# Kernel tuning notes

Hardware: AMD Instinct MI355X
Metric: run time of the kernel (lower is better)

The kernel has to match this reference:

```python
import jax, jax.numpy as jnp
import numpy as np

N_PART = 2048
N_BINS = 16
N_FREQS = 8
N_BLOCKS = 4
N_HEADS = 8
DIM = 256
HID = 512
LOWER = 0.0
UPPER = 1.0
FIXED_IDXS = np.array([0, 1])
CHANGED_IDXS = np.array([2])
N_FIXED = 2
N_CHANGED = 1
EMB_IN = 2 * N_FREQS * N_FIXED + 3   # 35
AFF_OUT = N_CHANGED * (3 * N_BINS + 1)  # 49
MIN_BIN = 1e-4
MIN_SLOPE = 1e-4


def _mlp(x, W0, b0, W1, b1, W2, b2):
    # equinox MLP: depth=2 hidden layers, relu activation, identity final
    x = jax.nn.relu(x @ W0.T + b0)
    x = jax.nn.relu(x @ W1.T + b1)
    return x @ W2.T + b2


def _attention(x, Wq, Wk, bk, Wv, Wo, bo):
    # eqx.nn.MultiheadAttention: query bias off, key bias on, value bias off, output bias on
    S, D = x.shape
    dh = D // N_HEADS
    q = (x @ Wq.T).reshape(S, N_HEADS, dh)
    k = (x @ Wk.T + bk).reshape(S, N_HEADS, dh)
    v = (x @ Wv.T).reshape(S, N_HEADS, dh)
    logits = jnp.einsum('shd,thd->hst', q, k) / float(np.sqrt(dh))
    attn = jax.nn.softmax(logits, axis=-1)
    o = jnp.einsum('hst,thd->shd', attn, v).reshape(S, D)
    return o @ Wo.T + bo


def _circular(x, lower, upper, n_freqs):
    # periodic sin/cos embedding of coordinates on [lower, upper)
    freqs = 2.0 * jnp.pi * jnp.arange(1, n_freqs + 1, dtype=x.dtype) / (upper - lower)
    ang = (x - lower)[..., None] * freqs  # (rows, n_fixed, n_freqs)
    feats = jnp.concatenate([jnp.cos(ang), jnp.sin(ang)], axis=-1)
    return feats.reshape(x.shape[0], -1)  # (rows, 2*n_freqs*n_fixed)


def _rqs_forward(x, params):
    # distrax-style rational quadratic spline, boundary_slopes='circular'
    nb = N_BINS
    uw = params[..., :nb]
    uh = params[..., nb:2 * nb]
    ud = params[..., 2 * nb:]
    ud = jnp.concatenate([ud[..., :-1], ud[..., :1]], axis=-1)  # circular: last slope = first
    total = UPPER - LOWER
    widths = jax.nn.softmax(uw, axis=-1) * (total - nb * MIN_BIN) + MIN_BIN
    heights = jax.nn.softmax(uh, axis=-1) * (total - nb * MIN_BIN) + MIN_BIN
    offset = float(np.log(np.expm1(1.0 - MIN_SLOPE)))  # softplus(0+offset)+min = 1
    slopes = jax.nn.softplus(ud + offset) + MIN_SLOPE
    zero = jnp.zeros(widths.shape[:-1] + (1,), widths.dtype)
    xpos = LOWER + jnp.concatenate([zero, jnp.cumsum(widths, -1)], -1)   # (..., nb+1)
    ypos = LOWER + jnp.concatenate([zero, jnp.cumsum(heights, -1)], -1)
    inside = (x >= LOWER) & (x <= UPPER)
    xc = jnp.clip(x, LOWER, UPPER)
    k = jnp.clip(jnp.sum(xc[..., None] >= xpos, axis=-1) - 1, 0, nb - 1)
    g = lambda a: jnp.take_along_axis(a, k[..., None], axis=-1)[..., 0]
    xk, xk1 = g(xpos[..., :-1]), g(xpos[..., 1:])
    yk, yk1 = g(ypos[..., :-1]), g(ypos[..., 1:])
    dk, dk1 = g(slopes[..., :-1]), g(slopes[..., 1:])
    w = xk1 - xk
    h = yk1 - yk
    s = h / w
    z = (xc - xk) / w
    z1 = 1.0 - z
    den = s + (dk1 + dk - 2.0 * s) * z * z1
    y = yk + h * (s * z * z + dk * z * z1) / den
    logdet = 2.0 * jnp.log(s) + jnp.log(dk1 * z * z + 2.0 * s * z * z1 + dk * z1 * z1) - 2.0 * jnp.log(den)
    y = jnp.where(inside, y, x)
    logdet = jnp.where(inside, logdet, 0.0)
    return y, logdet


def _forward(pos, scale, press, temp,
             e_w0, e_b0, e_w1, e_b1, e_w2, e_b2,
             Wq, Wk, bk, Wv, Wo, bo,
             mw0, mb0, mw1, mb1, mw2, mb2,
             a_w0, a_b0, a_w1, a_b1, a_w2, a_b2):
    fixed = pos[1:, FIXED_IDXS]      # (N-1, 2)
    changed = pos[1:, CHANGED_IDXS]  # (N-1, 1)
    feats = _circular(fixed[:, FIXED_IDXS], LOWER, UPPER, N_FREQS)  # (N-1, 32)
    rows = feats.shape[0]
    ones = jnp.ones((rows, 1), feats.dtype)
    cond = jnp.concatenate([feats, ones * scale, ones * temp, ones * press], axis=-1)  # (N-1, 35)
    h = _mlp(cond, e_w0, e_b0, e_w1, e_b1, e_w2, e_b2)  # (N-1, DIM)
    for i in range(N_BLOCKS):
        h = h + _attention(h, Wq[i], Wk[i], bk[i], Wv[i], Wo[i], bo[i])
        h = h + _mlp(h, mw0[i], mb0[i], mw1[i], mb1[i], mw2[i], mb2[i])
    params = _mlp(h, a_w0, a_b0, a_w1, a_b1, a_w2, a_b2)
    params = params.reshape(N_PART - 1, N_CHANGED, 3 * N_BINS + 1)
    y, logdet = _rqs_forward(changed, params)
    pos = pos.at[1:, CHANGED_IDXS].set(y.reshape(N_PART - 1, N_CHANGED))
    return pos, logdet.sum()


def setup_inputs():
    kit = iter(jax.random.split(jax.random.key(0), 40))
    nk = lambda: next(kit)
    def W(out_d, in_d, pre=()):
        return jax.random.normal(nk(), pre + (out_d, in_d), jnp.float32) / np.sqrt(in_d)
    def b(out_d, pre=()):
        return 0.01 * jax.random.normal(nk(), pre + (out_d,), jnp.float32)
    B = (N_BLOCKS,)
    return dict(
        pos=jax.random.uniform(nk(), (N_PART, 3), jnp.float32),
        scale=jax.random.uniform(nk(), (), jnp.float32),
        press=jax.random.uniform(nk(), (), jnp.float32),
        temp=jax.random.uniform(nk(), (), jnp.float32),
        e_w0=W(HID, EMB_IN), e_b0=b(HID),
        e_w1=W(HID, HID), e_b1=b(HID),
        e_w2=W(DIM, HID), e_b2=b(DIM),
        Wq=W(DIM, DIM, B), Wk=W(DIM, DIM, B), bk=b(DIM, B),
        Wv=W(DIM, DIM, B), Wo=W(DIM, DIM, B), bo=b(DIM, B),
        mw0=W(HID, DIM, B), mb0=b(HID, B),
        mw1=W(HID, HID, B), mb1=b(HID, B),
        mw2=W(DIM, HID, B), mb2=b(DIM, B),
        a_w0=W(HID, DIM), a_b0=b(HID),
        a_w1=W(HID, HID), a_b1=b(HID),
        a_w2=W(AFF_OUT, HID), a_b2=b(AFF_OUT),
    )


def reference(pos, scale, press, temp,
              e_w0, e_b0, e_w1, e_b1, e_w2, e_b2,
              Wq, Wk, bk, Wv, Wo, bo,
              mw0, mb0, mw1, mb1, mw2, mb2,
              a_w0, a_b0, a_w1, a_b1, a_w2, a_b2):
    return _forward(pos, scale, press, temp,
                    e_w0, e_b0, e_w1, e_b1, e_w2, e_b2,
                    Wq, Wk, bk, Wv, Wo, bo,
                    mw0, mb0, mw1, mb1, mw2, mb2,
                    a_w0, a_b0, a_w1, a_b1, a_w2, a_b2)
```

## Files before the change

kernel.cpp:

```cpp
#include <hip/hip_runtime.h>
#include <math.h>

#define S_ROWS 2047
#define DIM 256
#define HID 512
#define NHEADS 8
#define DH 32
#define NBINS 16
#define AFF_OUT 49

typedef short bf16x8 __attribute__((ext_vector_type(8)));
typedef float f32x4 __attribute__((ext_vector_type(4)));
typedef float f32x16 __attribute__((ext_vector_type(16)));
typedef unsigned short u16x8 __attribute__((ext_vector_type(8)));
typedef unsigned short u16x4 __attribute__((ext_vector_type(4)));

__device__ inline unsigned short f2b(float f) {
    unsigned int u = __float_as_uint(f);
    u += 0x7FFFu + ((u >> 16) & 1u);
    return (unsigned short)(u >> 16);
}

#define W_MAIN 3957248
#define EW0P_N 32768
#define P0 (W_MAIN / 4)
#define P1 (P0 + EW0P_N / 4)
#define P2 (P1 + 2048 * 64 / 4)
#define P3 (P2 + 1537)
__global__ __launch_bounds__(256) void setup_kernel(
    const float* __restrict__ pos, const float* __restrict__ scale,
    const float* __restrict__ press, const float* __restrict__ temp,
    const float* __restrict__ e_w0, const float* __restrict__ p0,
    const float* __restrict__ p1, const float* __restrict__ p2,
    const float* __restrict__ p3, const float* __restrict__ p4,
    const float* __restrict__ p5, const float* __restrict__ p6,
    const float* __restrict__ p7, const float* __restrict__ p8,
    const float* __restrict__ p9, const float* __restrict__ p10,
    const float* __restrict__ p11, unsigned short* __restrict__ dst,
    unsigned short* __restrict__ cond, float* __restrict__ out)
{
    const int offs[13] = {0, 262144, 393216, 655360, 917504, 1179648, 1441792,
                          1966080, 3014656, 3538944, 3670016, 3932160, 3957248};
    const float* srcs[12] = {p0,p1,p2,p3,p4,p5,p6,p7,p8,p9,p10,p11};
    for (int i4 = blockIdx.x * blockDim.x + threadIdx.x; i4 < P3;
         i4 += gridDim.x * blockDim.x) {
        if (i4 < P0) {
            int e = i4 * 4;
            int s = 0;
            #pragma unroll
            for (int j = 1; j < 12; j++) s += (e >= offs[j]);
            const float4 v = *(const float4*)(srcs[s] + (e - offs[s]));
            u16x4 o;
            o[0] = f2b(v.x); o[1] = f2b(v.y); o[2] = f2b(v.z); o[3] = f2b(v.w);
            *(u16x4*)(dst + EW0P_N + e) = o;
        } else if (i4 < P1) {
            int e = (i4 - P0) * 4;
            u16x4 o;
            #pragma unroll
            for (int r = 0; r < 4; r++) {
                int ee = e + r;
                int row = ee >> 6, col = ee & 63;
                o[r] = (col < 35) ? f2b(e_w0[row * 35 + col]) : (unsigned short)0;
            }
            *(u16x4*)(dst + e) = o;
        } else if (i4 < P2) {
            int e = (i4 - P1) * 4;
            int row = e >> 6;
            u16x4 o;
            #pragma unroll
            for (int r = 0; r < 4; r++) {
                int c = (e + r) & 63;
                float v = 0.f;
                if (row < S_ROWS) {
                    if (c < 32) {
                        int coord = c >> 4;
                        int w = c & 15;
                        float x = pos[(row + 1) * 3 + coord];
                        float f = 6.283185307179586f * (float)((w & 7) + 1);
                        float ang = x * f;
                        v = (w < 8) ? cosf(ang) : sinf(ang);
                    } else if (c == 32) v = scale[0];
                    else if (c == 33) v = temp[0];
                    else if (c == 34) v = press[0];
                }
                o[r] = f2b(v);
            }
            *(u16x4*)(cond + e) = o;
        } else {
            int e = (i4 - P2) * 4;
            #pragma unroll
            for (int r = 0; r < 4; r++) {
                int ee = e + r;
                if (ee < 6144) out[ee] = pos[ee];
                else if (ee == 6144) out[ee] = 0.f;
            }
        }
    }
}

#define LDK 72
__global__ __launch_bounds__(256, 2) void gemm_bf16(
    const unsigned short* __restrict__ Ab, const unsigned short* __restrict__ W,
    const float* __restrict__ bias, const float* resF,
    float* Cf, unsigned short* Cb, int M, int K, int relu)
{
    __shared__ unsigned short As[64][LDK];
    __shared__ unsigned short Bs[32][LDK];
    int tid = threadIdx.x;
    int wave = tid >> 6, lane = tid & 63;
    int quad = lane >> 4, l16 = lane & 15;
    int row0 = blockIdx.y << 6, col0 = blockIdx.x << 5;
    int srow = tid >> 2, scol = (tid & 3) << 4;
    int srowB = tid >> 3, scolB = (tid & 7) << 3;

    f32x4 acc[2];
    #pragma unroll
    for (int i = 0; i < 2; i++) { f32x4 z = {0.f,0.f,0.f,0.f}; acc[i] = z; }

    const u16x8* ap = (const u16x8*)(Ab + (size_t)(row0 + srow) * K + scol);
    const u16x8* wp = (const u16x8*)(W + (size_t)(col0 + srowB) * K + scolB);
    u16x8 a0 = ap[0], a1 = ap[1];
    u16x8 b0 = wp[0];

    for (int k0 = 0; k0 < K; k0 += 64) {
        *(u16x8*)&As[srow][scol]     = a0;
        *(u16x8*)&As[srow][scol + 8] = a1;
        *(u16x8*)&Bs[srowB][scolB]   = b0;
        __syncthreads();
        if (k0 + 64 < K) {
            ap += 8; wp += 8;
            a0 = ap[0]; a1 = ap[1];
            b0 = wp[0];
        }
        #pragma unroll
        for (int kt = 0; kt < 64; kt += 32) {
            bf16x8 af = *(bf16x8*)&As[(wave << 4) + l16][kt + (quad << 3)];
            #pragma unroll
            for (int n0 = 0; n0 < 2; n0++) {
                bf16x8 bf = *(bf16x8*)&Bs[(n0 << 4) + l16][kt + (quad << 3)];
                acc[n0] = __builtin_amdgcn_mfma_f32_16x16x32_bf16(af, bf, acc[n0], 0, 0, 0);
            }
        }
        __syncthreads();
    }
    #pragma unroll
    for (int n0 = 0; n0 < 2; n0++) {
        int col = col0 + (n0 << 4) + l16;
        if (col >= M) continue;
        float bv = bias ? bias[col] : 0.f;
        #pragma unroll
        for (int r = 0; r < 4; r++) {
            int row = row0 + (wave << 4) + (quad << 2) + r;
            if (row >= S_ROWS) continue;
            float v = acc[n0][r] + bv;
            if (resF) v += resF[(size_t)row * M + col];
            if (relu) v = fmaxf(v, 0.f);
            if (Cf) Cf[(size_t)row * M + col] = v;
            if (Cb) Cb[(size_t)row * M + col] = f2b(v);
        }
    }
}

__global__ __launch_bounds__(256, 2) void gemm_qkv(
    const unsigned short* __restrict__ Ab, const unsigned short* __restrict__ Wq,
    const unsigned short* __restrict__ Wk, const unsigned short* __restrict__ Wv,
    const float* __restrict__ bk,
    unsigned short* __restrict__ qbh, unsigned short* __restrict__ kbh,
    unsigned short* __restrict__ vbT)
{
    __shared__ unsigned short As[64][LDK];
    __shared__ unsigned short Bs[32][LDK];
    const int N = S_ROWS, K = 256;
    int tid = threadIdx.x;
    int wave = tid >> 6, lane = tid & 63;
    int quad = lane >> 4, l16 = lane & 15;
    int row0 = blockIdx.y << 6, col0 = blockIdx.x << 5;
    int mode = col0 >> 8;
    int wcol0 = col0 & 255;
    const unsigned short* W = (mode == 0) ? Wq : (mode == 1) ? Wk : Wv;
    int srow = tid >> 2, scol = (tid & 3) << 4;
    int srowB = tid >> 3, scolB = (tid & 7) << 3;

    f32x4 acc[2];
    #pragma unroll
    for (int i = 0; i < 2; i++) { f32x4 z = {0.f,0.f,0.f,0.f}; acc[i] = z; }

    const u16x8* ap = (const u16x8*)(Ab + (size_t)(row0 + srow) * K + scol);
    const u16x8* wp = (const u16x8*)(W + (size_t)(wcol0 + srowB) * K + scolB);
    u16x8 a0 = ap[0], a1 = ap[1];
    u16x8 b0 = wp[0];

    for (int k0 = 0; k0 < K; k0 += 64) {
        *(u16x8*)&As[srow][scol]     = a0;
        *(u16x8*)&As[srow][scol + 8] = a1;
        *(u16x8*)&Bs[srowB][scolB]   = b0;
        __syncthreads();
        if (k0 + 64 < K) {
            ap += 8; wp += 8;
            a0 = ap[0]; a1 = ap[1];
            b0 = wp[0];
        }
        #pragma unroll
        for (int kt = 0; kt < 64; kt += 32) {
            bf16x8 af = *(bf16x8*)&As[(wave << 4) + l16][kt + (quad << 3)];
            #pragma unroll
            for (int n0 = 0; n0 < 2; n0++) {
                bf16x8 bf = *(bf16x8*)&Bs[(n0 << 4) + l16][kt + (quad << 3)];
                acc[n0] = __builtin_amdgcn_mfma_f32_16x16x32_bf16(af, bf, acc[n0], 0, 0, 0);
            }
        }
        __syncthreads();
    }
    #pragma unroll
    for (int n0 = 0; n0 < 2; n0++) {
        int colr = wcol0 + (n0 << 4) + l16;
        int hh = colr >> 5, d = colr & 31;
        int rbase = row0 + (wave << 4) + (quad << 2);
        if (mode == 2) {
            unsigned short* dst = vbT + ((size_t)hh * 32 + d) * 2048 + rbase;
            if (rbase + 3 < N) {
                u16x4 o;
                #pragma unroll
                for (int r = 0; r < 4; r++) o[r] = f2b(acc[n0][r]);
                *(u16x4*)dst = o;
            } else {
                #pragma unroll
                for (int r = 0; r < 4; r++)
                    if (rbase + r < N) dst[r] = f2b(acc[n0][r]);
            }
        } else {
            float bias = (mode == 1) ? bk[colr] : 0.f;
            unsigned short* dst = ((mode == 0) ? qbh : kbh) + (size_t)hh * 2048 * 32 + d;
            #pragma unroll
            for (int r = 0; r < 4; r++) {
                int row = rbase + r;
                if (row < N) {
                    float v = acc[n0][r] + bias;
                    if (mode == 0) v *= 0.25506362f;
                    dst[(size_t)row * 32] = f2b(v);
                }
            }
        }
    }
}

__global__ __launch_bounds__(256, 2) void attn_mfma(
    const unsigned short* __restrict__ qbh,
    const unsigned short* __restrict__ kbh,
    const unsigned short* __restrict__ vbT,
    unsigned short* __restrict__ obb)
{
    int tid = threadIdx.x;
    int w = tid >> 6;
    int lane = tid & 63;
    int l31 = lane & 31, hf = lane >> 5;
    int q0 = blockIdx.x << 5;
    int h = blockIdx.y;
    int kstart = w * 512;
    int kend = min(kstart + 512, S_ROWS);

    const unsigned short* qp = qbh + ((size_t)h * 2048 + (q0 + l31)) * 32 + hf * 8;
    bf16x8 qf0 = *(const bf16x8*)(qp);
    bf16x8 qf1 = *(const bf16x8*)(qp + 16);

    const unsigned short* kb_h = kbh + (size_t)h * 2048 * 32;
    const unsigned short* vb_h = vbT + ((size_t)h * 32 + l31) * 2048;

    f32x16 acc = {};
    float m = -1e30f, l = 0.f;

    for (int key0 = kstart; key0 < kend; key0 += 32) {
        const unsigned short* kp = kb_h + (size_t)(key0 + l31) * 32 + hf * 8;
        bf16x8 kf0 = *(const bf16x8*)(kp);
        bf16x8 kf1 = *(const bf16x8*)(kp + 16);
        bf16x8 vf0 = *(const bf16x8*)(vb_h + key0 + hf * 8);
        bf16x8 vf1 = *(const bf16x8*)(vb_h + key0 + 16 + hf * 8);

        f32x16 sc = {};
        sc = __builtin_amdgcn_mfma_f32_32x32x16_bf16(kf0, qf0, sc, 0, 0, 0);
        sc = __builtin_amdgcn_mfma_f32_32x32x16_bf16(kf1, qf1, sc, 0, 0, 0);

        if (key0 + 32 > kend) {
            #pragma unroll
            for (int r = 0; r < 16; r++) {
                int kr = key0 + (r & 3) + 8 * (r >> 2) + 4 * hf;
                if (kr >= kend) sc[r] = -1e30f;
            }
        }
        float tmax = sc[0];
        #pragma unroll
        for (int r = 1; r < 16; r++) tmax = fmaxf(tmax, sc[r]);
        tmax = fmaxf(tmax, __shfl_xor(tmax, 32, 64));
        float mnew = fmaxf(m, tmax);
        float corr = __builtin_amdgcn_exp2f(m - mnew);
        m = mnew;
        float p[16];
        float ls = 0.f;
        #pragma unroll
        for (int r = 0; r < 16; r++) {
            p[r] = __builtin_amdgcn_exp2f(sc[r] - mnew);
            ls += p[r];
        }
        ls += __shfl_xor(ls, 32, 64);
        l = l * corr + ls;
        if (__ballot(corr != 1.0f)) {
            #pragma unroll
            for (int r = 0; r < 16; r++) acc[r] *= corr;
        }
        unsigned int pk[8];
        #pragma unroll
        for (int i = 0; i < 8; i++)
            pk[i] = __builtin_amdgcn_perm(__float_as_uint(p[2*i+1]),
                                          __float_as_uint(p[2*i]), 0x07060302u);
        unsigned int x[8];
        #pragma unroll
        for (int i = 0; i < 8; i++)
            x[i] = (unsigned int)__shfl_xor((int)pk[i], 32, 64);
        union { unsigned int u[4]; bf16x8 v; } B1, B2;
        B1.u[0] = hf ? x[2]  : pk[0];
        B1.u[1] = hf ? x[3]  : pk[1];
        B1.u[2] = hf ? pk[2] : x[0];
        B1.u[3] = hf ? pk[3] : x[1];
        B2.u[0] = hf ? x[6]  : pk[4];
        B2.u[1] = hf ? x[7]  : pk[5];
        B2.u[2] = hf ? pk[6] : x[4];
        B2.u[3] = hf ? pk[7] : x[5];
        acc = __builtin_amdgcn_mfma_f32_32x32x16_bf16(vf0, B1.v, acc, 0, 0, 0);
        acc = __builtin_amdgcn_mfma_f32_32x32x16_bf16(vf1, B2.v, acc, 0, 0, 0);
    }

    __shared__ float sm_m[4][32];
    __shared__ float sm_l[4][32];
    __shared__ float sm_acc[4][32][36];
    if (!hf) { sm_m[w][l31] = m; sm_l[w][l31] = l; }
    #pragma unroll
    for (int g = 0; g < 4; g++) {
        float4 o4;
        o4.x = acc[4*g]; o4.y = acc[4*g+1]; o4.z = acc[4*g+2]; o4.w = acc[4*g+3];
        *(float4*)&sm_acc[w][l31][8*g + 4*hf] = o4;
    }
    __syncthreads();

    int q = tid & 31;
    int dg = tid >> 5;
    float mmax = fmaxf(fmaxf(sm_m[0][q], sm_m[1][q]),
                       fmaxf(sm_m[2][q], sm_m[3][q]));
    float lsum = 0.f;
    float num0 = 0.f, num1 = 0.f, num2 = 0.f, num3 = 0.f;
    #pragma unroll
    for (int c = 0; c < 4; c++) {
        float wgt = __builtin_amdgcn_exp2f(sm_m[c][q] - mmax);
        lsum += sm_l[c][q] * wgt;
        float4 o4 = *(const float4*)&sm_acc[c][q][dg * 4];
        num0 = fmaf(o4.x, wgt, num0);
        num1 = fmaf(o4.y, wgt, num1);
        num2 = fmaf(o4.z, wgt, num2);
        num3 = fmaf(o4.w, wgt, num3);
    }
    float inv = 1.f / lsum;
    if (q0 + q < S_ROWS) {
        u16x4 st;
        st[0] = f2b(num0 * inv); st[1] = f2b(num1 * inv);
        st[2] = f2b(num2 * inv); st[3] = f2b(num3 * inv);
        *(u16x4*)(obb + (size_t)(q0 + q) * DIM + h * DH + dg * 4) = st;
    }
}

__global__ __launch_bounds__(64) void spline_kernel(const float* __restrict__ pos,
    const float* __restrict__ params, float* __restrict__ out)
{
    int r = blockIdx.x * 64 + threadIdx.x;
    float ld = 0.f;
    if (r < S_ROWS) {
        const float* p = params + (size_t)r * AFF_OUT;
        float x = pos[(r + 1) * 3 + 2];
        float xc = fminf(fmaxf(x, 0.f), 1.f);

        float mw = -1e30f, mh = -1e30f;
        #pragma unroll
        for (int j = 0; j < NBINS; j++) {
            mw = fmaxf(mw, p[j]);
            mh = fmaxf(mh, p[NBINS + j]);
        }
        float sw = 0.f, sh = 0.f;
        #pragma unroll
        for (int j = 0; j < NBINS; j++) {
            sw += __expf(p[j] - mw);
            sh += __expf(p[NBINS + j] - mh);
        }
        const float span = 1.0f - NBINS * 1e-4f;
        float scw = span / sw, sch = span / sh;

        float cumw = 0.f, cumh = 0.f;
        float xk = 0.f, yk = 0.f, wk = 0.f, hk = 0.f;
        int k = 0;
        #pragma unroll
        for (int j = 0; j < NBINS; j++) {
            float wj = __expf(p[j] - mw) * scw + 1e-4f;
            float hj = __expf(p[NBINS + j] - mh) * sch + 1e-4f;
            if (xc >= cumw) { k = j; xk = cumw; yk = cumh; wk = wj; hk = hj; }
            cumw += wj; cumh += hj;
        }
        float offset = logf(expm1f(0.9999f));
        float t0 = p[2 * NBINS + k] + offset;
        float t1 = ((k == NBINS - 1) ? p[2 * NBINS] : p[2 * NBINS + k + 1]) + offset;
        float dk  = ((t0 > 15.f) ? t0 : log1pf(__expf(t0))) + 1e-4f;
        float dk1 = ((t1 > 15.f) ? t1 : log1pf(__expf(t1))) + 1e-4f;

        float sl = hk / wk;
        float z = (xc - xk) / wk;
        float z1 = 1.f - z;
        float den = sl + (dk1 + dk - 2.f * sl) * z * z1;
        float y = yk + hk * (sl * z * z + dk * z * z1) / den;
        float ldv = 2.f * logf(sl)
                  + logf(dk1 * z * z + 2.f * sl * z * z1 + dk * z1 * z1)
                  - 2.f * logf(den);
        bool inside = (x >= 0.f) && (x <= 1.f);
        y = inside ? y : x;
        ld = inside ? ldv : 0.f;
        out[(r + 1) * 3 + 2] = y;
    }
    #pragma unroll
    for (int st = 32; st > 0; st >>= 1) ld += __shfl_xor(ld, st, 64);
    if (threadIdx.x == 0) atomicAdd(&out[6144], ld);
}

extern "C" void kernel_launch(void* const* d_in, const int* in_sizes, int n_in,
                              void* d_out, int out_size, void* d_ws, size_t ws_size,
                              hipStream_t stream)
{
    const float* pos   = (const float*)d_in[0];
    const float* scale = (const float*)d_in[1];
    const float* press = (const float*)d_in[2];
    const float* temp  = (const float*)d_in[3];
    const float* e_w0  = (const float*)d_in[4];
    const float* e_b0  = (const float*)d_in[5];
    const float* e_w1  = (const float*)d_in[6];
    const float* e_b1  = (const float*)d_in[7];
    const float* e_w2  = (const float*)d_in[8];
    const float* e_b2  = (const float*)d_in[9];
    const float* Wq    = (const float*)d_in[10];
    const float* Wk    = (const float*)d_in[11];
    const float* bk    = (const float*)d_in[12];
    const float* Wv    = (const float*)d_in[13];
    const float* Wo    = (const float*)d_in[14];
    const float* bo    = (const float*)d_in[15];
    const float* mw0   = (const float*)d_in[16];
    const float* mb0   = (const float*)d_in[17];
    const float* mw1   = (const float*)d_in[18];
    const float* mb1   = (const float*)d_in[19];
    const float* mw2   = (const float*)d_in[20];
    const float* mb2   = (const float*)d_in[21];
    const float* a_w0  = (const float*)d_in[22];
    const float* a_b0  = (const float*)d_in[23];
    const float* a_w1  = (const float*)d_in[24];
    const float* a_b1  = (const float*)d_in[25];
    const float* a_w2  = (const float*)d_in[26];
    const float* a_b2  = (const float*)d_in[27];
    float* out = (float*)d_out;

    enum { OFF_EW0 = 0,
           OFF_EW1 = 32768 + 0,       OFF_EW2 = 32768 + 262144,
           OFF_WQ  = 32768 + 393216,  OFF_WK  = 32768 + 655360,
           OFF_WV  = 32768 + 917504,  OFF_WO  = 32768 + 1179648,
           OFF_MW0 = 32768 + 1441792, OFF_MW1 = 32768 + 1966080,
           OFF_MW2 = 32768 + 3014656, OFF_AW0 = 32768 + 3538944,
           OFF_AW1 = 32768 + 3670016, OFF_AW2 = 32768 + 3932160 };
    const size_t WB_U16 = (size_t)EW0P_N + W_MAIN;

    float* ws = (float*)d_ws;
    size_t off = 0;
    float* hbuf = ws + off; off += 2048 * 256;
    float* pr   = ws + off; off += 2048 * 64;
    unsigned short* wbp   = (unsigned short*)(ws + off); off += WB_U16 / 2;
    unsigned short* cond  = (unsigned short*)(ws + off); off += 2048 * 64 / 2;
    unsigned short* t1b   = (unsigned short*)(ws + off); off += 2048 * 512 / 2;
    unsigned short* t2b   = (unsigned short*)(ws + off); off += 2048 * 512 / 2;
    unsigned short* hb    = (unsigned short*)(ws + off); off += 2048 * 256 / 2;
    unsigned short* obb   = (unsigned short*)(ws + off); off += 2048 * 256 / 2;
    unsigned short* qbh   = (unsigned short*)(ws + off); off += NHEADS * 2048 * 32 / 2;
    unsigned short* kbh   = (unsigned short*)(ws + off); off += NHEADS * 2048 * 32 / 2;
    unsigned short* vbT   = (unsigned short*)(ws + off); off += NHEADS * 2048 * 32 / 2;
    (void)ws_size;

    dim3 b256(256);
    hipLaunchKernelGGL(setup_kernel, dim3(1024), b256, 0, stream,
                       pos, scale, press, temp, e_w0,
                       e_w1, e_w2, Wq, Wk, Wv, Wo, mw0, mw1, mw2,
                       a_w0, a_w1, a_w2, wbp, cond, out);

    auto gemm = [&](const unsigned short* A, const unsigned short* W,
                    const float* bias, const float* resF, float* Cf,
                    unsigned short* Cb, int M, int K, int relu) {
        dim3 grid((M + 31) / 32, 32);
        hipLaunchKernelGGL(gemm_bf16, grid, dim3(256), 0, stream,
                           A, W, bias, resF, Cf, Cb, M, K, relu);
    };

    gemm(cond, wbp + OFF_EW0, e_b0, nullptr, nullptr, t1b, 512, 64, 1);
    gemm(t1b,  wbp + OFF_EW1, e_b1, nullptr, nullptr, t2b, 512, 512, 1);
    gemm(t2b,  wbp + OFF_EW2, e_b2, nullptr, hbuf, hb, 256, 512, 0);

    for (int l = 0; l < 4; l++) {
        hipLaunchKernelGGL(gemm_qkv, dim3(24, 32), b256, 0, stream,
                           hb, wbp + OFF_WQ + l * 65536, wbp + OFF_WK + l * 65536,
                           wbp + OFF_WV + l * 65536, bk + l * 256, qbh, kbh, vbT);
        hipLaunchKernelGGL(attn_mfma, dim3(64, NHEADS), b256, 0, stream,
                           qbh, kbh, vbT, obb);
        gemm(obb, wbp + OFF_WO + l * 65536, bo + l * 256, hbuf, hbuf, hb, 256, 256, 0);
        gemm(hb,  wbp + OFF_MW0 + l * 131072, mb0 + l * 512, nullptr, nullptr, t1b, 512, 256, 1);
        gemm(t1b, wbp + OFF_MW1 + l * 262144, mb1 + l * 512, nullptr, nullptr, t2b, 512, 512, 1);
        gemm(t2b, wbp + OFF_MW2 + l * 131072, mb2 + l * 256, hbuf, hbuf, hb, 256, 512, 0);
    }

    gemm(hb,  wbp + OFF_AW0, a_b0, nullptr, nullptr, t1b, 512, 256, 1);
    gemm(t1b, wbp + OFF_AW1, a_b1, nullptr, nullptr, t2b, 512, 512, 1);
    gemm(t2b, wbp + OFF_AW2, a_b2, nullptr, pr, nullptr, AFF_OUT, 512, 0);

    hipLaunchKernelGGL(spline_kernel, dim3(32), dim3(64), 0, stream, pos, pr, out);
}
```

Before: 359.8 us.

## Fuse per-row MLP chains into single LDS-resident kernel per layer

Replaces the separate tiled GEMM launches (embedding MLP, QKV projection, output projection, block MLP, affine MLP, spline) with one chain kernel. Each 16-row block keeps activations and the residual stream in shared memory across consecutive linear layers, and streams weights directly from global memory into MFMA operands. This cuts kernel launches and the global round-trips of intermediate activations, leaving only attention as a separate kernel. In exchange, only 128 blocks of 512 threads run, and weights are re-read by every block without LDS staging, which may lower occupancy and raise weight traffic.

Result: slower. 441.2 us (+22.6%).

```diff
diff --git a/kernel.cpp b/kernel.cpp
--- a/kernel.cpp
+++ b/kernel.cpp
@@ -20,6 +20,20 @@
     u += 0x7FFFu + ((u >> 16) & 1u);
     return (unsigned short)(u >> 16);
 }
+
+#define OFF_EW0 0
+#define OFF_EW1 (32768 + 0)
+#define OFF_EW2 (32768 + 262144)
+#define OFF_WQ  (32768 + 393216)
+#define OFF_WK  (32768 + 655360)
+#define OFF_WV  (32768 + 917504)
+#define OFF_WO  (32768 + 1179648)
+#define OFF_MW0 (32768 + 1441792)
+#define OFF_MW1 (32768 + 1966080)
+#define OFF_MW2 (32768 + 3014656)
+#define OFF_AW0 (32768 + 3538944)
+#define OFF_AW1 (32768 + 3670016)
+#define OFF_AW2 (32768 + 3932160)
 
 #define W_MAIN 3957248
 #define EW0P_N 32768
@@ -98,135 +112,78 @@
     }
 }
 
-#define LDK 72
-__global__ __launch_bounds__(256, 2) void gemm_bf16(
-    const unsigned short* __restrict__ Ab, const unsigned short* __restrict__ W,
-    const float* __restrict__ bias, const float* resF,
-    float* Cf, unsigned short* Cb, int M, int K, int relu)
-{
-    __shared__ unsigned short As[64][LDK];
-    __shared__ unsigned short Bs[32][LDK];
-    int tid = threadIdx.x;
-    int wave = tid >> 6, lane = tid & 63;
-    int quad = lane >> 4, l16 = lane & 15;
-    int row0 = blockIdx.y << 6, col0 = blockIdx.x << 5;
-    int srow = tid >> 2, scol = (tid & 3) << 4;
-    int srowB = tid >> 3, scolB = (tid & 7) << 3;
-
-    f32x4 acc[2];
-    #pragma unroll
-    for (int i = 0; i < 2; i++) { f32x4 z = {0.f,0.f,0.f,0.f}; acc[i] = z; }
-
-    const u16x8* ap = (const u16x8*)(Ab + (size_t)(row0 + srow) * K + scol);
-    const u16x8* wp = (const u16x8*)(W + (size_t)(col0 + srowB) * K + scolB);
-    u16x8 a0 = ap[0], a1 = ap[1];
-    u16x8 b0 = wp[0];
-
-    for (int k0 = 0; k0 < K; k0 += 64) {
-        *(u16x8*)&As[srow][scol]     = a0;
-        *(u16x8*)&As[srow][scol + 8] = a1;
-        *(u16x8*)&Bs[srowB][scolB]   = b0;
-        __syncthreads();
-        if (k0 + 64 < K) {
-            ap += 8; wp += 8;
-            a0 = ap[0]; a1 = ap[1];
-            b0 = wp[0];
-        }
-        #pragma unroll
-        for (int kt = 0; kt < 64; kt += 32) {
-            bf16x8 af = *(bf16x8*)&As[(wave << 4) + l16][kt + (quad << 3)];
-            #pragma unroll
-            for (int n0 = 0; n0 < 2; n0++) {
-                bf16x8 bf = *(bf16x8*)&Bs[(n0 << 4) + l16][kt + (quad << 3)];
-                acc[n0] = __builtin_amdgcn_mfma_f32_16x16x32_bf16(af, bf, acc[n0], 0, 0, 0);
-            }
-        }
-        __syncthreads();
-    }
-    #pragma unroll
-    for (int n0 = 0; n0 < 2; n0++) {
-        int col = col0 + (n0 << 4) + l16;
-        if (col >= M) continue;
-        float bv = bias ? bias[col] : 0.f;
+#define LDA 520
+#define LDR 260
+
+template<int K, bool RELU, int RESMODE>
+__device__ inline void stage_lds(
+    const unsigned short (*IN)[LDA], unsigned short (*OUT)[LDA],
+    float (*res)[LDR],
+    const unsigned short* __restrict__ W, const float* __restrict__ bias,
+    int M, int wave, int quad, int l16)
+{
+    bf16x8 af[K / 32];
+    #pragma unroll
+    for (int i = 0; i < K / 32; i++)
+        af[i] = *(const bf16x8*)&IN[l16][(i << 5) + (quad << 3)];
+    for (int m0 = wave << 4; m0 < M; m0 += 128) {
+        const unsigned short* wp = W + (size_t)(m0 + l16) * K + (quad << 3);
+        f32x4 acc = {0.f, 0.f, 0.f, 0.f};
+        #pragma unroll
+        for (int i = 0; i < K / 32; i++) {
+            bf16x8 bf = *(const bf16x8*)(wp + (i << 5));
+            acc = __builtin_amdgcn_mfma_f32_16x16x32_bf16(af[i], bf, acc, 0, 0, 0);
+        }
+        int col = m0 + l16;
+        float bv = bias[col];
         #pragma unroll
         for (int r = 0; r < 4; r++) {
-            int row = row0 + (wave << 4) + (quad << 2) + r;
-            if (row >= S_ROWS) continue;
-            float v = acc[n0][r] + bv;
-            if (resF) v += resF[(size_t)row * M + col];
-            if (relu) v = fmaxf(v, 0.f);
-            if (Cf) Cf[(size_t)row * M + col] = v;
-            if (Cb) Cb[(size_t)row * M + col] = f2b(v);
-        }
-    }
-}
-
-__global__ __launch_bounds__(256, 2) void gemm_qkv(
-    const unsigned short* __restrict__ Ab, const unsigned short* __restrict__ Wq,
-    const unsigned short* __restrict__ Wk, const unsigned short* __restrict__ Wv,
-    const float* __restrict__ bk,
+            int row = (quad << 2) + r;
+            float v = acc[r] + bv;
+            if (RESMODE == 1) { v += res[row][col]; res[row][col] = v; }
+            if (RESMODE == 2) { res[row][col] = v; }
+            if (RELU) v = fmaxf(v, 0.f);
+            OUT[row][col] = f2b(v);
+        }
+    }
+}
+
+__device__ inline void stage_qkv(
+    const unsigned short (*IN)[LDA],
+    const unsigned short* __restrict__ Wq, const unsigned short* __restrict__ Wk,
+    const unsigned short* __restrict__ Wv, const float* __restrict__ bk,
     unsigned short* __restrict__ qbh, unsigned short* __restrict__ kbh,
-    unsigned short* __restrict__ vbT)
-{
-    __shared__ unsigned short As[64][LDK];
-    __shared__ unsigned short Bs[32][LDK];
-    const int N = S_ROWS, K = 256;
-    int tid = threadIdx.x;
-    int wave = tid >> 6, lane = tid & 63;
-    int quad = lane >> 4, l16 = lane & 15;
-    int row0 = blockIdx.y << 6, col0 = blockIdx.x << 5;
-    int mode = col0 >> 8;
-    int wcol0 = col0 & 255;
-    const unsigned short* W = (mode == 0) ? Wq : (mode == 1) ? Wk : Wv;
-    int srow = tid >> 2, scol = (tid & 3) << 4;
-    int srowB = tid >> 3, scolB = (tid & 7) << 3;
-
-    f32x4 acc[2];
-    #pragma unroll
-    for (int i = 0; i < 2; i++) { f32x4 z = {0.f,0.f,0.f,0.f}; acc[i] = z; }
-
-    const u16x8* ap = (const u16x8*)(Ab + (size_t)(row0 + srow) * K + scol);
-    const u16x8* wp = (const u16x8*)(W + (size_t)(wcol0 + srowB) * K + scolB);
-    u16x8 a0 = ap[0], a1 = ap[1];
-    u16x8 b0 = wp[0];
-
-    for (int k0 = 0; k0 < K; k0 += 64) {
-        *(u16x8*)&As[srow][scol]     = a0;
-        *(u16x8*)&As[srow][scol + 8] = a1;
-        *(u16x8*)&Bs[srowB][scolB]   = b0;
-        __syncthreads();
-        if (k0 + 64 < K) {
-            ap += 8; wp += 8;
-            a0 = ap[0]; a1 = ap[1];
-            b0 = wp[0];
-        }
-        #pragma unroll
-        for (int kt = 0; kt < 64; kt += 32) {
-            bf16x8 af = *(bf16x8*)&As[(wave << 4) + l16][kt + (quad << 3)];
-            #pragma unroll
-            for (int n0 = 0; n0 < 2; n0++) {
-                bf16x8 bf = *(bf16x8*)&Bs[(n0 << 4) + l16][kt + (quad << 3)];
-                acc[n0] = __builtin_amdgcn_mfma_f32_16x16x32_bf16(af, bf, acc[n0], 0, 0, 0);
-            }
-        }
-        __syncthreads();
-    }
-    #pragma unroll
-    for (int n0 = 0; n0 < 2; n0++) {
-        int colr = wcol0 + (n0 << 4) + l16;
+    unsigned short* __restrict__ vbT,
+    int row0, int wave, int quad, int l16)
+{
+    bf16x8 af[8];
+    #pragma unroll
+    for (int i = 0; i < 8; i++)
+        af[i] = *(const bf16x8*)&IN[l16][(i << 5) + (quad << 3)];
+    for (int m0 = wave << 4; m0 < 768; m0 += 128) {
+        int mode = m0 >> 8, wcol0 = m0 & 255;
+        const unsigned short* W = (mode == 0) ? Wq : (mode == 1) ? Wk : Wv;
+        const unsigned short* wp = W + (size_t)(wcol0 + l16) * 256 + (quad << 3);
+        f32x4 acc = {0.f, 0.f, 0.f, 0.f};
+        #pragma unroll
+        for (int i = 0; i < 8; i++) {
+            bf16x8 bf = *(const bf16x8*)(wp + (i << 5));
+            acc = __builtin_amdgcn_mfma_f32_16x16x32_bf16(af[i], bf, acc, 0, 0, 0);
+        }
+        int colr = wcol0 + l16;
         int hh = colr >> 5, d = colr & 31;
-        int rbase = row0 + (wave << 4) + (quad << 2);
+        int rbase = row0 + (quad << 2);
         if (mode == 2) {
             unsigned short* dst = vbT + ((size_t)hh * 32 + d) * 2048 + rbase;
-            if (rbase + 3 < N) {
+            if (rbase + 3 < S_ROWS) {
                 u16x4 o;
                 #pragma unroll
-                for (int r = 0; r < 4; r++) o[r] = f2b(acc[n0][r]);
+                for (int r = 0; r < 4; r++) o[r] = f2b(acc[r]);
                 *(u16x4*)dst = o;
             } else {
                 #pragma unroll
                 for (int r = 0; r < 4; r++)
-                    if (rbase + r < N) dst[r] = f2b(acc[n0][r]);
+                    if (rbase + r < S_ROWS) dst[r] = f2b(acc[r]);
             }
         } else {
             float bias = (mode == 1) ? bk[colr] : 0.f;
@@ -234,11 +191,176 @@
             #pragma unroll
             for (int r = 0; r < 4; r++) {
                 int row = rbase + r;
-                if (row < N) {
-                    float v = acc[n0][r] + bias;
+                if (row < S_ROWS) {
+                    float v = acc[r] + bias;
                     if (mode == 0) v *= 0.25506362f;
                     dst[(size_t)row * 32] = f2b(v);
                 }
+            }
+        }
+    }
+}
+
+__device__ inline float spline_row(const float* p, float x, float* yout)
+{
+    float xc = fminf(fmaxf(x, 0.f), 1.f);
+    float mw = -1e30f, mh = -1e30f;
+    #pragma unroll
+    for (int j = 0; j < NBINS; j++) {
+        mw = fmaxf(mw, p[j]);
+        mh = fmaxf(mh, p[NBINS + j]);
+    }
+    float sw = 0.f, shs = 0.f;
+    #pragma unroll
+    for (int j = 0; j < NBINS; j++) {
+        sw += __expf(p[j] - mw);
+        shs += __expf(p[NBINS + j] - mh);
+    }
+    const float span = 1.0f - NBINS * 1e-4f;
+    float scw = span / sw, sch = span / shs;
+    float cumw = 0.f, cumh = 0.f;
+    float xk = 0.f, yk = 0.f, wk = 0.f, hk = 0.f;
+    int k = 0;
+    #pragma unroll
+    for (int j = 0; j < NBINS; j++) {
+        float wj = __expf(p[j] - mw) * scw + 1e-4f;
+        float hj = __expf(p[NBINS + j] - mh) * sch + 1e-4f;
+        if (xc >= cumw) { k = j; xk = cumw; yk = cumh; wk = wj; hk = hj; }
+        cumw += wj; cumh += hj;
+    }
+    float offset = logf(expm1f(0.9999f));
+    float t0 = p[2 * NBINS + k] + offset;
+    float t1 = ((k == NBINS - 1) ? p[2 * NBINS] : p[2 * NBINS + k + 1]) + offset;
+    float dk  = ((t0 > 15.f) ? t0 : log1pf(__expf(t0))) + 1e-4f;
+    float dk1 = ((t1 > 15.f) ? t1 : log1pf(__expf(t1))) + 1e-4f;
+    float sl = hk / wk;
+    float z = (xc - xk) / wk;
+    float z1 = 1.f - z;
+    float den = sl + (dk1 + dk - 2.f * sl) * z * z1;
+    float y = yk + hk * (sl * z * z + dk * z * z1) / den;
+    float ldv = 2.f * logf(sl)
+              + logf(dk1 * z * z + 2.f * sl * z * z1 + dk * z1 * z1)
+              - 2.f * logf(den);
+    bool inside = (x >= 0.f) && (x <= 1.f);
+    *yout = inside ? y : x;
+    return inside ? ldv : 0.f;
+}
+
+__global__ __launch_bounds__(512, 2) void chain_kernel(
+    int mode,
+    const unsigned short* __restrict__ wbp,
+    const unsigned short* __restrict__ cond,
+    const unsigned short* __restrict__ obb,
+    float* __restrict__ hbuf,
+    unsigned short* __restrict__ qbh, unsigned short* __restrict__ kbh,
+    unsigned short* __restrict__ vbT,
+    const float* __restrict__ e_b0, const float* __restrict__ e_b1,
+    const float* __restrict__ e_b2,
+    const float* __restrict__ bo, const float* __restrict__ mb0,
+    const float* __restrict__ mb1, const float* __restrict__ mb2,
+    const float* __restrict__ bk,
+    const float* __restrict__ a_b0, const float* __restrict__ a_b1,
+    const float* __restrict__ a_b2,
+    const float* __restrict__ pos, float* __restrict__ out)
+{
+    __shared__ unsigned short actA[16][LDA];
+    __shared__ unsigned short actB[16][LDA];
+    __shared__ float res[16][LDR];
+    __shared__ float pl[16][52];
+
+    int tid = threadIdx.x;
+    int wave = tid >> 6, lane = tid & 63;
+    int quad = lane >> 4, l16 = lane & 15;
+    int row0 = blockIdx.x << 4;
+
+    if (mode < 0) {
+        if (tid < 128) {
+            int r = tid >> 3, c = (tid & 7) << 3;
+            *(u16x8*)&actA[r][c] = *(const u16x8*)(cond + (size_t)(row0 + r) * 64 + c);
+        }
+        __syncthreads();
+        stage_lds<64, true, 0>(actA, actB, res, wbp + OFF_EW0, e_b0, 512, wave, quad, l16);
+        __syncthreads();
+        stage_lds<512, true, 0>(actB, actA, res, wbp + OFF_EW1, e_b1, 512, wave, quad, l16);
+        __syncthreads();
+        stage_lds<512, false, 2>(actA, actB, res, wbp + OFF_EW2, e_b2, 256, wave, quad, l16);
+        __syncthreads();
+        {
+            int r = tid >> 5, c = (tid & 31) << 3;
+            *(float4*)(hbuf + (size_t)(row0 + r) * 256 + c)     = *(float4*)&res[r][c];
+            *(float4*)(hbuf + (size_t)(row0 + r) * 256 + c + 4) = *(float4*)&res[r][c + 4];
+        }
+        stage_qkv(actB, wbp + OFF_WQ, wbp + OFF_WK, wbp + OFF_WV, bk,
+                  qbh, kbh, vbT, row0, wave, quad, l16);
+    } else {
+        int l = mode;
+        {
+            int r = tid >> 5, c = (tid & 31) << 3;
+            *(u16x8*)&actA[r][c] = *(const u16x8*)(obb + (size_t)(row0 + r) * 256 + c);
+            *(float4*)&res[r][c]     = *(const float4*)(hbuf + (size_t)(row0 + r) * 256 + c);
+            *(float4*)&res[r][c + 4] = *(const float4*)(hbuf + (size_t)(row0 + r) * 256 + c + 4);
+        }
+        __syncthreads();
+        stage_lds<256, false, 1>(actA, actB, res, wbp + OFF_WO + l * 65536,
+                                 bo + l * 256, 256, wave, quad, l16);
+        __syncthreads();
+        stage_lds<256, true, 0>(actB, actA, res, wbp + OFF_MW0 + l * 131072,
+                                mb0 + l * 512, 512, wave, quad, l16);
+        __syncthreads();
+        stage_lds<512, true, 0>(actA, actB, res, wbp + OFF_MW1 + l * 262144,
+                                mb1 + l * 512, 512, wave, quad, l16);
+        __syncthreads();
+        stage_lds<512, false, 1>(actB, actA, res, wbp + OFF_MW2 + l * 131072,
+                                 mb2 + l * 256, 256, wave, quad, l16);
+        __syncthreads();
+        if (l < 3) {
+            {
+                int r = tid >> 5, c = (tid & 31) << 3;
+                *(float4*)(hbuf + (size_t)(row0 + r) * 256 + c)     = *(float4*)&res[r][c];
+                *(float4*)(hbuf + (size_t)(row0 + r) * 256 + c + 4) = *(float4*)&res[r][c + 4];
+            }
+            stage_qkv(actA, wbp + OFF_WQ + (l + 1) * 65536, wbp + OFF_WK + (l + 1) * 65536,
+                      wbp + OFF_WV + (l + 1) * 65536, bk + (l + 1) * 256,
+                      qbh, kbh, vbT, row0, wave, quad, l16);
+        } else {
+            stage_lds<256, true, 0>(actA, actB, res, wbp + OFF_AW0, a_b0, 512, wave, quad, l16);
+            __syncthreads();
+            stage_lds<512, true, 0>(actB, actA, res, wbp + OFF_AW1, a_b1, 512, wave, quad, l16);
+            __syncthreads();
+            if (wave < 4) {
+                bf16x8 af[16];
+                #pragma unroll
+                for (int i = 0; i < 16; i++)
+                    af[i] = *(const bf16x8*)&actA[l16][(i << 5) + (quad << 3)];
+                int m0 = wave << 4;
+                const unsigned short* wp = wbp + OFF_AW2 + (size_t)(m0 + l16) * 512 + (quad << 3);
+                f32x4 acc = {0.f, 0.f, 0.f, 0.f};
+                #pragma unroll
+                for (int i = 0; i < 16; i++) {
+                    bf16x8 bf = *(const bf16x8*)(wp + (i << 5));
+                    acc = __builtin_amdgcn_mfma_f32_16x16x32_bf16(af[i], bf, acc, 0, 0, 0);
+                }
+                int col = m0 + l16;
+                if (col < AFF_OUT) {
+                    float bv = a_b2[col];
+                    #pragma unroll
+                    for (int r = 0; r < 4; r++)
+                        pl[(quad << 2) + r][col] = acc[r] + bv;
+                }
+            }
+            __syncthreads();
+            if (tid < 16) {
+                float ld = 0.f;
+                int grow = row0 + tid;
+                if (grow < S_ROWS) {
+                    float x = pos[(grow + 1) * 3 + 2];
+                    float y;
+                    ld = spline_row(&pl[tid][0], x, &y);
+                    out[(grow + 1) * 3 + 2] = y;
+                }
+                #pragma unroll
+                for (int st = 8; st > 0; st >>= 1) ld += __shfl_xor(ld, st, 64);
+                if (tid == 0) atomicAdd(&out[6144], ld);
             }
         }
     }
@@ -364,65 +486,6 @@
         st[2] = f2b(num2 * inv); st[3] = f2b(num3 * inv);
         *(u16x4*)(obb + (size_t)(q0 + q) * DIM + h * DH + dg * 4) = st;
     }
-}
-
-__global__ __launch_bounds__(64) void spline_kernel(const float* __restrict__ pos,
-    const float* __restrict__ params, float* __restrict__ out)
-{
-    int r = blockIdx.x * 64 + threadIdx.x;
-    float ld = 0.f;
-    if (r < S_ROWS) {
-        const float* p = params + (size_t)r * AFF_OUT;
-        float x = pos[(r + 1) * 3 + 2];
-        float xc = fminf(fmaxf(x, 0.f), 1.f);
-
-        float mw = -1e30f, mh = -1e30f;
-        #pragma unroll
-        for (int j = 0; j < NBINS; j++) {
-            mw = fmaxf(mw, p[j]);
-            mh = fmaxf(mh, p[NBINS + j]);
-        }
-        float sw = 0.f, sh = 0.f;
-        #pragma unroll
-        for (int j = 0; j < NBINS; j++) {
-            sw += __expf(p[j] - mw);
-            sh += __expf(p[NBINS + j] - mh);
-        }
-        const float span = 1.0f - NBINS * 1e-4f;
-        float scw = span / sw, sch = span / sh;
-
-        float cumw = 0.f, cumh = 0.f;
-        float xk = 0.f, yk = 0.f, wk = 0.f, hk = 0.f;
-        int k = 0;
-        #pragma unroll
-        for (int j = 0; j < NBINS; j++) {
-            float wj = __expf(p[j] - mw) * scw + 1e-4f;
-            float hj = __expf(p[NBINS + j] - mh) * sch + 1e-4f;
-            if (xc >= cumw) { k = j; xk = cumw; yk = cumh; wk = wj; hk = hj; }
-            cumw += wj; cumh += hj;
-        }
-        float offset = logf(expm1f(0.9999f));
-        float t0 = p[2 * NBINS + k] + offset;
-        float t1 = ((k == NBINS - 1) ? p[2 * NBINS] : p[2 * NBINS + k + 1]) + offset;
-        float dk  = ((t0 > 15.f) ? t0 : log1pf(__expf(t0))) + 1e-4f;
-        float dk1 = ((t1 > 15.f) ? t1 : log1pf(__expf(t1))) + 1e-4f;
-
-        float sl = hk / wk;
-        float z = (xc - xk) / wk;
-        float z1 = 1.f - z;
-        float den = sl + (dk1 + dk - 2.f * sl) * z * z1;
-        float y = yk + hk * (sl * z * z + dk * z * z1) / den;
-        float ldv = 2.f * logf(sl)
-                  + logf(dk1 * z * z + 2.f * sl * z * z1 + dk * z1 * z1)
-                  - 2.f * logf(den);
-        bool inside = (x >= 0.f) && (x <= 1.f);
-        y = inside ? y : x;
-        ld = inside ? ldv : 0.f;
-        out[(r + 1) * 3 + 2] = y;
-    }
-    #pragma unroll
-    for (int st = 32; st > 0; st >>= 1) ld += __shfl_xor(ld, st, 64);
-    if (threadIdx.x == 0) atomicAdd(&out[6144], ld);
 }
 
 extern "C" void kernel_launch(void* const* d_in, const int* in_sizes, int n_in,
@@ -459,63 +522,35 @@
     const float* a_b2  = (const float*)d_in[27];
     float* out = (float*)d_out;
 
-    enum { OFF_EW0 = 0,
-           OFF_EW1 = 32768 + 0,       OFF_EW2 = 32768 + 262144,
-           OFF_WQ  = 32768 + 393216,  OFF_WK  = 32768 + 655360,
-           OFF_WV  = 32768 + 917504,  OFF_WO  = 32768 + 1179648,
-           OFF_MW0 = 32768 + 1441792, OFF_MW1 = 32768 + 1966080,
-           OFF_MW2 = 32768 + 3014656, OFF_AW0 = 32768 + 3538944,
-           OFF_AW1 = 32768 + 3670016, OFF_AW2 = 32768 + 3932160 };
     const size_t WB_U16 = (size_t)EW0P_N + W_MAIN;
 
     float* ws = (float*)d_ws;
     size_t off = 0;
     float* hbuf = ws + off; off += 2048 * 256;
-    float* pr   = ws + off; off += 2048 * 64;
     unsigned short* wbp   = (unsigned short*)(ws + off); off += WB_U16 / 2;
     unsigned short* cond  = (unsigned short*)(ws + off); off += 2048 * 64 / 2;
-    unsigned short* t1b   = (unsigned short*)(ws + off); off += 2048 * 512 / 2;
-    unsigned short* t2b   = (unsigned short*)(ws + off); off += 2048 * 512 / 2;
-    unsigned short* hb    = (unsigned short*)(ws + off); off += 2048 * 256 / 2;
     unsigned short* obb   = (unsigned short*)(ws + off); off += 2048 * 256 / 2;
     unsigned short* qbh   = (unsigned short*)(ws + off); off += NHEADS * 2048 * 32 / 2;
     unsigned short* kbh   = (unsigned short*)(ws + off); off += NHEADS * 2048 * 32 / 2;
     unsigned short* vbT   = (unsigned short*)(ws + off); off += NHEADS * 2048 * 32 / 2;
     (void)ws_size;
 
-    dim3 b256(256);
-    hipLaunchKernelGGL(setup_kernel, dim3(1024), b256, 0, stream,
+    hipLaunchKernelGGL(setup_kernel, dim3(1024), dim3(256), 0, stream,
                        pos, scale, press, temp, e_w0,
                        e_w1, e_w2, Wq, Wk, Wv, Wo, mw0, mw1, mw2,
                        a_w0, a_w1, a_w2, wbp, cond, out);
 
-    auto gemm = [&](const unsigned short* A, const unsigned short* W,
-                    const float* bias, const float* resF, float* Cf,
-                    unsigned short* Cb, int M, int K, int relu) {
-        dim3 grid((M + 31) / 32, 32);
-        hipLaunchKernelGGL(gemm_bf16, grid, dim3(256), 0, stream,
-                           A, W, bias, resF, Cf, Cb, M, K, relu);
+    auto chain = [&](int mode) {
+        hipLaunchKernelGGL(chain_kernel, dim3(128), dim3(512), 0, stream,
+                           mode, wbp, cond, obb, hbuf, qbh, kbh, vbT,
+                           e_b0, e_b1, e_b2, bo, mb0, mb1, mb2, bk,
+                           a_b0, a_b1, a_b2, pos, out);
     };
 
-    gemm(cond, wbp + OFF_EW0, e_b0, nullptr, nullptr, t1b, 512, 64, 1);
-    gemm(t1b,  wbp + OFF_EW1, e_b1, nullptr, nullptr, t2b, 512, 512, 1);
-    gemm(t2b,  wbp + OFF_EW2, e_b2, nullptr, hbuf, hb, 256, 512, 0);
-
+    chain(-1);
     for (int l = 0; l < 4; l++) {
-        hipLaunchKernelGGL(gemm_qkv, dim3(24, 32), b256, 0, stream,
-                           hb, wbp + OFF_WQ + l * 65536, wbp + OFF_WK + l * 65536,
-                           wbp + OFF_WV + l * 65536, bk + l * 256, qbh, kbh, vbT);
-        hipLaunchKernelGGL(attn_mfma, dim3(64, NHEADS), b256, 0, stream,
+        hipLaunchKernelGGL(attn_mfma, dim3(64, NHEADS), dim3(256), 0, stream,
                            qbh, kbh, vbT, obb);
-        gemm(obb, wbp + OFF_WO + l * 65536, bo + l * 256, hbuf, hbuf, hb, 256, 256, 0);
-        gemm(hb,  wbp + OFF_MW0 + l * 131072, mb0 + l * 512, nullptr, nullptr, t1b, 512, 256, 1);
-        gemm(t1b, wbp + OFF_MW1 + l * 262144, mb1 + l * 512, nullptr, nullptr, t2b, 512, 512, 1);
-        gemm(t2b, wbp + OFF_MW2 + l * 131072, mb2 + l * 256, hbuf, hbuf, hb, 256, 512, 0);
-    }
-
-    gemm(hb,  wbp + OFF_AW0, a_b0, nullptr, nullptr, t1b, 512, 256, 1);
-    gemm(t1b, wbp + OFF_AW1, a_b1, nullptr, nullptr, t2b, 512, 512, 1);
-    gemm(t2b, wbp + OFF_AW2, a_b2, nullptr, pr, nullptr, AFF_OUT, 512, 0);
-
-    hipLaunchKernelGGL(spline_kernel, dim3(32), dim3(64), 0, stream, pos, pr, out);
-}
+        chain(l);
+    }
+}
```
